# Optimization experiments

Hardware: AMD Instinct MI355X
Metric: run time of the kernel (lower is better)

## Reference

```python
import jax, jax.numpy as jnp
import numpy as np

HIDDEN = 4096
N_HEADS = 32
N_KV = 32
HEAD_DIM = 128
T = 2048
EPS = 1e-5
ROPE_THETA = 1000000.0


def rms_norm(x, w, eps=EPS):
    var = jnp.mean(x * x, axis=-1, keepdims=True)
    return x * jax.lax.rsqrt(var + eps) * w


def apply_rope(x, positions):
    # x: [T, H, D] ; neox-style (rotate halves), full rotary_dim = HEAD_DIM
    half = HEAD_DIM // 2
    inv_freq = 1.0 / (ROPE_THETA ** (jnp.arange(0, half, dtype=jnp.float32) / half))
    ang = positions.astype(jnp.float32)[:, None] * inv_freq  # [T, half]
    cos = jnp.cos(ang)[:, None, :]  # [T, 1, half]
    sin = jnp.sin(ang)[:, None, :]
    x1, x2 = x[..., :half], x[..., half:]
    return jnp.concatenate([x1 * cos - x2 * sin, x2 * cos + x1 * sin], axis=-1)


def setup_inputs() -> dict:
    key = jax.random.key(0)
    ks = jax.random.split(key, 5)
    s = 0.02
    qkv_out = (N_HEADS + 2 * N_KV) * HEAD_DIM
    return {
        "hidden_states": jax.random.normal(ks[0], (T, HIDDEN), jnp.float32),
        "positions": jnp.arange(T, dtype=jnp.int32),
        "w_qkv": jax.random.normal(ks[1], (qkv_out, HIDDEN), jnp.float32) * s,
        "b_qkv": jax.random.normal(ks[2], (qkv_out,), jnp.float32) * s,
        "q_norm_w": jnp.ones((N_HEADS * HEAD_DIM,), jnp.float32),
        "k_norm_w": jnp.ones((N_KV * HEAD_DIM,), jnp.float32),
        "w_o": jax.random.normal(ks[3], (HIDDEN, N_HEADS * HEAD_DIM), jnp.float32) * s,
    }


def reference(hidden_states, positions, w_qkv, b_qkv, q_norm_w, k_norm_w, w_o):
    q_size = N_HEADS * HEAD_DIM
    kv_size = N_KV * HEAD_DIM
    qkv = hidden_states @ w_qkv.T + b_qkv  # [T, q+2kv]
    q, k, v = jnp.split(qkv, [q_size, q_size + kv_size], axis=-1)
    # QK RMSNorm over the full flattened q / k widths (as in Molmo)
    q = rms_norm(q, q_norm_w)
    k = rms_norm(k, k_norm_w)
    q = apply_rope(q.reshape(T, N_HEADS, HEAD_DIM), positions)
    k = apply_rope(k.reshape(T, N_KV, HEAD_DIM), positions)
    v = v.reshape(T, N_KV, HEAD_DIM)
    scale = HEAD_DIM ** -0.5
    scores = jnp.einsum("qhd,khd->hqk", q, k) * scale  # [H, T, T]
    causal = positions[:, None] >= positions[None, :]
    scores = jnp.where(causal[None], scores, jnp.float32(-1e30))
    probs = jax.nn.softmax(scores, axis=-1)
    attn = jnp.einsum("hqk,khd->qhd", probs, v).reshape(T, N_HEADS * HEAD_DIM)
    return attn @ w_o.T
```

## Files before the change

kernel.cpp:

```cpp
#include <hip/hip_runtime.h>
#include <hip/hip_bf16.h>

#define T_SEQ 2048
#define NH 32
#define HD 128
#define QKV_N 12288
#define V_OFF 8192

typedef __bf16 bf16;
typedef __attribute__((ext_vector_type(4))) __bf16 bf16x4;
typedef __attribute__((ext_vector_type(8))) __bf16 bf16x8;
typedef __attribute__((ext_vector_type(4))) float f32x4;

#define GLDS16(g, l)                                                        \
  __builtin_amdgcn_global_load_lds(                                         \
      (const __attribute__((address_space(1))) void*)(g),                   \
      (__attribute__((address_space(3))) void*)(l), 16, 0, 0)

__device__ inline bf16x8 load8(const bf16* p) { return *(const bf16x8*)p; }
__device__ inline bf16x8 load8(const float* p) {
    f32x4 a = *(const f32x4*)p;
    f32x4 b = *(const f32x4*)(p + 4);
    bf16x8 r;
    r[0] = (bf16)a[0]; r[1] = (bf16)a[1]; r[2] = (bf16)a[2]; r[3] = (bf16)a[3];
    r[4] = (bf16)b[0]; r[5] = (bf16)b[1]; r[6] = (bf16)b[2]; r[7] = (bf16)b[3];
    return r;
}

__global__ __launch_bounds__(256)
void f32_to_bf16(const float* __restrict__ in, bf16* __restrict__ out, int n8)
{
    for (int i = blockIdx.x * 256 + threadIdx.x; i < n8; i += gridDim.x * 256)
        *(bf16x8*)(out + (size_t)i * 8) = load8(in + (size_t)i * 8);
}

template <typename TO>
__global__ __launch_bounds__(512, 2)
void gemm_bt_p1(const bf16* __restrict__ A, int lda,
                const bf16* __restrict__ B,
                const float* __restrict__ bias,
                TO* __restrict__ C, int ldc,
                int mTiles, int colPerXcd, int K)
{
    __shared__ char lds[98304];
    char* ldsA = lds;
    char* ldsB = lds + 65536;

    const int tid  = threadIdx.x;
    const int wave = tid >> 6, lane = tid & 63;
    const int quad = lane >> 4, l16 = lane & 15;
    const int wm = wave >> 1, wn = wave & 1;

    const int b   = blockIdx.x;
    const int xcd = b & 7, i = b >> 3;
    const int rowBase = (i % mTiles) * 256;
    const int colBase = (xcd * colPerXcd + i / mTiles) * 128;
    const int nK = K >> 5;

    const bf16* gA0; const bf16* gA1; const bf16* gB0;
    {
        int d0 = tid * 16;
        int s0 = d0 ^ ((d0 >> 3) & 0x70);
        gA0 = A + (size_t)(rowBase + (s0 >> 6)) * lda + ((s0 & 63) >> 1);
        int d1 = (512 + tid) * 16;
        int s1 = d1 ^ ((d1 >> 3) & 0x70);
        gA1 = A + (size_t)(rowBase + (s1 >> 6)) * lda + ((s1 & 63) >> 1);
        int d2 = tid * 16;
        int s2 = d2 ^ ((d2 >> 3) & 0x70);
        gB0 = B + (size_t)(colBase + (s2 >> 6)) * K + ((s2 & 63) >> 1);
    }

    auto stage = [&](int kt) {
        const int sl = kt & 3;
        const int ko = kt * 32;
        GLDS16(gA0 + ko, ldsA + sl * 16384 + wave * 1024);
        GLDS16(gA1 + ko, ldsA + sl * 16384 + 8192 + wave * 1024);
        GLDS16(gB0 + ko, ldsB + sl * 8192 + wave * 1024);
    };

    int offA[4], offB[4];
#pragma unroll
    for (int mi = 0; mi < 4; ++mi) {
        int a = (wm * 64 + mi * 16 + l16) * 64 + quad * 16;
        offA[mi] = a ^ ((a >> 3) & 0x70);
    }
#pragma unroll
    for (int ni = 0; ni < 4; ++ni) {
        int a = (wn * 64 + ni * 16 + l16) * 64 + quad * 16;
        offB[ni] = a ^ ((a >> 3) & 0x70);
    }

    f32x4 acc[4][4] = {};

    stage(0); stage(1); stage(2);
    asm volatile("s_waitcnt vmcnt(6)" ::: "memory");
    __builtin_amdgcn_s_barrier();

#pragma unroll 4
    for (int kt = 0; kt < nK; ++kt) {
        const char* sA = ldsA + (kt & 3) * 16384;
        const char* sB = ldsB + (kt & 3) * 8192;
        bf16x8 af[4], bfr[4];
#pragma unroll
        for (int mi = 0; mi < 4; ++mi) af[mi]  = *(const bf16x8*)(sA + offA[mi]);
#pragma unroll
        for (int ni = 0; ni < 4; ++ni) bfr[ni] = *(const bf16x8*)(sB + offB[ni]);
        if (kt + 3 < nK) stage(kt + 3);
        __builtin_amdgcn_sched_barrier(0);
        __builtin_amdgcn_s_setprio(1);
#pragma unroll
        for (int mi = 0; mi < 4; ++mi)
#pragma unroll
            for (int ni = 0; ni < 4; ++ni)
                acc[mi][ni] = __builtin_amdgcn_mfma_f32_16x16x32_bf16(
                    af[mi], bfr[ni], acc[mi][ni], 0, 0, 0);
        __builtin_amdgcn_s_setprio(0);
        __builtin_amdgcn_sched_barrier(0);
        if (kt + 3 < nK) {
            asm volatile("s_waitcnt vmcnt(6)" ::: "memory");
            __builtin_amdgcn_s_barrier();
        } else if (kt + 2 < nK) {
            asm volatile("s_waitcnt vmcnt(3)" ::: "memory");
            __builtin_amdgcn_s_barrier();
        } else if (kt + 1 < nK) {
            asm volatile("s_waitcnt vmcnt(0)" ::: "memory");
            __builtin_amdgcn_s_barrier();
        }
    }

#pragma unroll
    for (int ni = 0; ni < 4; ++ni) {
        int col = colBase + wn * 64 + ni * 16 + l16;
        float bv = bias ? bias[col] : 0.0f;
#pragma unroll
        for (int mi = 0; mi < 4; ++mi) {
            int row0 = rowBase + wm * 64 + mi * 16 + quad * 4;
#pragma unroll
            for (int r = 0; r < 4; ++r)
                C[(size_t)(row0 + r) * ldc + col] = (TO)(acc[mi][ni][r] + bv);
        }
    }
}

#define BM 128
#define BN 128
#define BK 32

template <typename TA, typename TB, typename TO>
__global__ __launch_bounds__(256, 2)
void gemm_bt_bias(const TA* __restrict__ A, int lda,
                  const TB* __restrict__ B,
                  const float* __restrict__ bias,
                  TO* __restrict__ C, int ldc,
                  int M, int N, int K)
{
    __shared__ bf16 sA[BM * BK];
    __shared__ bf16 sB[BN * BK];
    const int tid  = threadIdx.x;
    const int wave = tid >> 6, lane = tid & 63;
    const int quad = lane >> 4, l16 = lane & 15;
    const int wm = wave >> 1, wn = wave & 1;
    const int rowBase = blockIdx.x * BM;
    const int colBase = blockIdx.y * BN;

    int c0 = wave * 128 + lane;
    int rowA0 = c0 >> 2, kgA0 = c0 & 3;
    int rowA1 = (c0 + 64) >> 2, kgA1 = (c0 + 64) & 3;

    f32x4 acc[4][4] = {};

    for (int k0 = 0; k0 < K; k0 += BK) {
        bf16x8 ra0 = load8(A + (size_t)(rowBase + rowA0) * lda + k0 + kgA0 * 8);
        bf16x8 ra1 = load8(A + (size_t)(rowBase + rowA1) * lda + k0 + kgA1 * 8);
        bf16x8 rb0 = load8(B + (size_t)(colBase + rowA0) * K + k0 + kgA0 * 8);
        bf16x8 rb1 = load8(B + (size_t)(colBase + rowA1) * K + k0 + kgA1 * 8);
        __syncthreads();
        *(bf16x8*)(sA + rowA0 * BK + kgA0 * 8) = ra0;
        *(bf16x8*)(sA + rowA1 * BK + kgA1 * 8) = ra1;
        *(bf16x8*)(sB + rowA0 * BK + kgA0 * 8) = rb0;
        *(bf16x8*)(sB + rowA1 * BK + kgA1 * 8) = rb1;
        __syncthreads();

        bf16x8 af[4], bfr[4];
        for (int mi = 0; mi < 4; ++mi)
            af[mi] = *(const bf16x8*)(sA + (wm * 64 + mi * 16 + l16) * BK + quad * 8);
        for (int ni = 0; ni < 4; ++ni)
            bfr[ni] = *(const bf16x8*)(sB + (wn * 64 + ni * 16 + l16) * BK + quad * 8);
        for (int mi = 0; mi < 4; ++mi)
            for (int ni = 0; ni < 4; ++ni)
                acc[mi][ni] = __builtin_amdgcn_mfma_f32_16x16x32_bf16(
                    af[mi], bfr[ni], acc[mi][ni], 0, 0, 0);
    }

    for (int ni = 0; ni < 4; ++ni) {
        int col = colBase + wn * 64 + ni * 16 + l16;
        float bv = bias ? bias[col] : 0.0f;
        for (int mi = 0; mi < 4; ++mi) {
            int row0 = rowBase + wm * 64 + mi * 16 + quad * 4;
            for (int r = 0; r < 4; ++r)
                C[(size_t)(row0 + r) * ldc + col] = (TO)(acc[mi][ni][r] + bv);
        }
    }
}

__global__ __launch_bounds__(256)
void rmsnorm_rope(bf16* __restrict__ qkv, const float* __restrict__ qw,
                  const float* __restrict__ kw, const int* __restrict__ pos)
{
    const int t   = blockIdx.x;
    const int sel = blockIdx.y;
    bf16* x = qkv + (size_t)t * QKV_N + sel * 4096;
    const float* w = sel ? kw : qw;
    const int tid = threadIdx.x;

    float ss = 0.f;
    {
        int i0 = tid * 16;
        bf16x8 a = *(const bf16x8*)(x + i0);
        bf16x8 b = *(const bf16x8*)(x + i0 + 8);
        for (int j = 0; j < 8; ++j) { float fa = (float)a[j]; ss += fa * fa; }
        for (int j = 0; j < 8; ++j) { float fb = (float)b[j]; ss += fb * fb; }
    }
    for (int off = 1; off < 64; off <<= 1) ss += __shfl_xor(ss, off, 64);
    __shared__ float red[4];
    if ((tid & 63) == 0) red[tid >> 6] = ss;
    __syncthreads();
    float tot = red[0] + red[1] + red[2] + red[3];
    float rstd = rsqrtf(tot * (1.0f / 4096.0f) + 1e-5f);

    float fp = (float)pos[t];
    for (int i = tid; i < 2048; i += 256) {
        int h = i >> 6;
        int d = i & 63;
        int base = h * 128 + d;
        float x1 = (float)x[base]      * rstd * w[base];
        float x2 = (float)x[base + 64] * rstd * w[base + 64];
        float ang = fp * exp2f(-(float)d * 0.31143075889569023f);
        float s, c;
        sincosf(ang, &s, &c);
        x[base]      = (bf16)(x1 * c - x2 * s);
        x[base + 64] = (bf16)(x2 * c + x1 * s);
    }
}

__global__ __launch_bounds__(256)
void v_transpose(const bf16* __restrict__ qkv, bf16* __restrict__ vt)
{
    __shared__ bf16 tile[64][65];
    int t0 = blockIdx.x * 64, d0 = blockIdx.y * 64, h = blockIdx.z;
    int x = threadIdx.x & 63, y4 = threadIdx.x >> 6;
    for (int yy = y4; yy < 64; yy += 4)
        tile[yy][x] = qkv[(size_t)(t0 + yy) * QKV_N + V_OFF + h * HD + d0 + x];
    __syncthreads();
    for (int yy = y4; yy < 64; yy += 4)
        vt[(size_t)(h * HD + d0 + yy) * T_SEQ + t0 + x] = tile[x][yy];
}

#define SKP 136
#define SVP 72
#define PBP 72

__global__ __launch_bounds__(256, 2)
void flash_attn(bf16* qkv, const bf16* vt)
{
    __shared__ bf16 sK[64 * SKP];
    __shared__ bf16 sV[128 * SVP];
    __shared__ bf16 pbuf[4 * 16 * PBP];

    const int tid  = threadIdx.x;
    const int wave = tid >> 6, lane = tid & 63;
    const int quad = lane >> 4, l16 = lane & 15;
    const int h    = blockIdx.y;

    const float sc = 0.08838834764831845f * 1.4426950408889634f;
    bf16* pb = pbuf + wave * 16 * PBP;

    for (int half = 0; half < 2; ++half) {
        const int blk  = half ? (31 - (int)blockIdx.x) : (int)blockIdx.x;
        const int q0w  = blk * 64 + wave * 16;
        const int kend = blk * 64;
        const int qln  = q0w + l16;

        bf16x8 qf[4];
        {
            const bf16* qrow = qkv + (size_t)qln * QKV_N + h * HD;
            for (int c = 0; c < 4; ++c)
                qf[c] = *(const bf16x8*)(qrow + c * 32 + quad * 8);
        }

        f32x4 oacc[8] = {};
        float m2 = -1e30f, lsum = 0.f;

        for (int kb = 0; kb <= kend; kb += 64) {
            __syncthreads();
            for (int j = 0; j < 4; ++j) {
                int c = tid + j * 256;
                int r = c >> 4, off = (c & 15) * 8;
                bf16x8 v = *(const bf16x8*)(qkv + (size_t)(kb + r) * QKV_N + 4096 + h * HD + off);
                *(bf16x8*)(sK + r * SKP + off) = v;
            }
            for (int j = 0; j < 4; ++j) {
                int c = tid + j * 256;
                int d = c >> 3, off = (c & 7) * 8;
                bf16x8 v = *(const bf16x8*)(vt + (size_t)(h * HD + d) * T_SEQ + kb + off);
                *(bf16x8*)(sV + d * SVP + off) = v;
            }
            __syncthreads();

            const int stmax = (kb == kend) ? (wave + 1) : 4;

            f32x4 s[4] = {};
            for (int st = 0; st < 4; ++st) {
                if (st >= stmax) break;
                const bf16* kbase = sK + (st * 16 + l16) * SKP + quad * 8;
                for (int c = 0; c < 4; ++c) {
                    bf16x8 kf = *(const bf16x8*)(kbase + c * 32);
                    s[st] = __builtin_amdgcn_mfma_f32_16x16x32_bf16(kf, qf[c], s[st], 0, 0, 0);
                }
            }
            for (int st = 0; st < 4; ++st) {
                int k0r = kb + st * 16 + quad * 4;
                for (int r = 0; r < 4; ++r) {
                    float v = s[st][r] * sc;
                    s[st][r] = (k0r + r <= qln) ? v : -1e30f;
                }
            }
            float mx = -1e30f;
            for (int st = 0; st < 4; ++st)
                for (int r = 0; r < 4; ++r) mx = fmaxf(mx, s[st][r]);
            mx = fmaxf(mx, __shfl_xor(mx, 16, 64));
            mx = fmaxf(mx, __shfl_xor(mx, 32, 64));
            float mnew  = fmaxf(m2, mx);
            float alpha = exp2f(m2 - mnew);
            float ps = 0.f;
            for (int st = 0; st < 4; ++st)
                for (int r = 0; r < 4; ++r) {
                    float p = exp2f(s[st][r] - mnew);
                    s[st][r] = p;
                    ps += p;
                }
            ps += __shfl_xor(ps, 16, 64);
            ps += __shfl_xor(ps, 32, 64);
            lsum = lsum * alpha + ps;
            m2 = mnew;

            float ar[4];
            for (int r = 0; r < 4; ++r) ar[r] = __shfl(alpha, quad * 4 + r, 64);
            for (int c = 0; c < 8; ++c)
                for (int r = 0; r < 4; ++r) oacc[c][r] *= ar[r];

            for (int st = 0; st < 4; ++st) {
                bf16x4 pw;
                for (int r = 0; r < 4; ++r) pw[r] = (bf16)s[st][r];
                *(bf16x4*)(pb + l16 * PBP + st * 16 + quad * 4) = pw;
            }
            __builtin_amdgcn_s_waitcnt(0xC07F);
            for (int ph = 0; ph < 2; ++ph) {
                bf16x8 pf = *(const bf16x8*)(pb + l16 * PBP + ph * 32 + quad * 8);
                for (int c = 0; c < 8; ++c) {
                    bf16x8 vf = *(const bf16x8*)(sV + (c * 16 + l16) * SVP + ph * 32 + quad * 8);
                    oacc[c] = __builtin_amdgcn_mfma_f32_16x16x32_bf16(pf, vf, oacc[c], 0, 0, 0);
                }
            }
        }

        float lr[4];
        for (int r = 0; r < 4; ++r) lr[r] = __shfl(lsum, quad * 4 + r, 64);
        for (int r = 0; r < 4; ++r) {
            float inv = 1.0f / lr[r];
            int t = q0w + quad * 4 + r;
            for (int c = 0; c < 8; ++c)
                qkv[(size_t)t * QKV_N + V_OFF + h * HD + c * 16 + l16] =
                    (bf16)(oacc[c][r] * inv);
        }
    }
}

extern "C" void kernel_launch(void* const* d_in, const int* in_sizes, int n_in,
                              void* d_out, int out_size, void* d_ws, size_t ws_size,
                              hipStream_t stream)
{
    const float* hidden   = (const float*)d_in[0];
    const int*   pos      = (const int*)d_in[1];
    const float* w_qkv    = (const float*)d_in[2];
    const float* b_qkv    = (const float*)d_in[3];
    const float* q_norm_w = (const float*)d_in[4];
    const float* k_norm_w = (const float*)d_in[5];
    const float* w_o      = (const float*)d_in[6];
    float* out = (float*)d_out;

    bf16* qkv = (bf16*)d_ws;
    bf16* vt  = qkv + (size_t)T_SEQ * QKV_N;
    bf16* wqb = vt  + (size_t)4096 * T_SEQ;
    bf16* wob = wqb + (size_t)QKV_N * 4096;
    bf16* hib = wob + (size_t)4096 * 4096;
    const size_t need = ((size_t)T_SEQ * QKV_N + (size_t)4096 * T_SEQ +
                         (size_t)QKV_N * 4096 + (size_t)4096 * 4096 +
                         (size_t)T_SEQ * 4096) * 2;

    if (ws_size >= need) {
        f32_to_bf16<<<2048, 256, 0, stream>>>(hidden, hib, T_SEQ * 4096 / 8);
        f32_to_bf16<<<8192, 256, 0, stream>>>(w_qkv, wqb, QKV_N * 4096 / 8);
        f32_to_bf16<<<4096, 256, 0, stream>>>(w_o, wob, 4096 * 4096 / 8);

        gemm_bt_p1<bf16><<<768, 512, 0, stream>>>(
            hib, 4096, wqb, b_qkv, qkv, QKV_N, 8, 12, 4096);
        rmsnorm_rope<<<dim3(T_SEQ, 2), 256, 0, stream>>>(qkv, q_norm_w, k_norm_w, pos);
        v_transpose<<<dim3(T_SEQ / 64, 2, NH), 256, 0, stream>>>(qkv, vt);
        flash_attn<<<dim3(T_SEQ / 128, NH), 256, 0, stream>>>(qkv, vt);
        gemm_bt_p1<float><<<256, 512, 0, stream>>>(
            qkv + V_OFF, QKV_N, wob, nullptr, out, 4096, 8, 4, 4096);
    } else {
        gemm_bt_bias<float, float, bf16><<<dim3(T_SEQ / BM, QKV_N / BN), 256, 0, stream>>>(
            hidden, 4096, w_qkv, b_qkv, qkv, QKV_N, T_SEQ, QKV_N, 4096);
        rmsnorm_rope<<<dim3(T_SEQ, 2), 256, 0, stream>>>(qkv, q_norm_w, k_norm_w, pos);
        v_transpose<<<dim3(T_SEQ / 64, 2, NH), 256, 0, stream>>>(qkv, vt);
        flash_attn<<<dim3(T_SEQ / 128, NH), 256, 0, stream>>>(qkv, vt);
        gemm_bt_bias<bf16, float, float><<<dim3(T_SEQ / BM, 4096 / BN), 256, 0, stream>>>(
            qkv + V_OFF, QKV_N, w_o, nullptr, out, 4096, T_SEQ, 4096, 4096);
    }
}
```

Measured before the change: 798.0 us.

## Shrink GEMM tile to 128x128 with 256 threads and double-buffered LDS

Replaces the 256x128-tile, 512-thread GEMM with a 4-stage LDS pipeline by a 128x128-tile, 256-thread kernel with 2-stage double buffering and 32KB LDS. Launch bounds and grid sizes change so more blocks run, giving 1536 and 512 blocks and up to 3 blocks per CU. The aim is better occupancy and CU coverage, especially for the smaller output projection, at the price of less data reuse per tile and a shallower prefetch that may expose more memory latency.

```diff
diff --git a/kernel.cpp b/kernel.cpp
--- a/kernel.cpp
+++ b/kernel.cpp
@@ -35,16 +35,14 @@
 }
 
 template <typename TO>
-__global__ __launch_bounds__(512, 2)
-void gemm_bt_p1(const bf16* __restrict__ A, int lda,
+__global__ __launch_bounds__(256, 3)
+void gemm_bt_cr(const bf16* __restrict__ A, int lda,
                 const bf16* __restrict__ B,
                 const float* __restrict__ bias,
                 TO* __restrict__ C, int ldc,
                 int mTiles, int colPerXcd, int K)
 {
-    __shared__ char lds[98304];
-    char* ldsA = lds;
-    char* ldsB = lds + 65536;
+    __shared__ char lds[32768];
 
     const int tid  = threadIdx.x;
     const int wave = tid >> 6, lane = tid & 63;
@@ -53,29 +51,29 @@
 
     const int b   = blockIdx.x;
     const int xcd = b & 7, i = b >> 3;
-    const int rowBase = (i % mTiles) * 256;
+    const int rowBase = (i % mTiles) * 128;
     const int colBase = (xcd * colPerXcd + i / mTiles) * 128;
     const int nK = K >> 5;
 
-    const bf16* gA0; const bf16* gA1; const bf16* gB0;
-    {
-        int d0 = tid * 16;
-        int s0 = d0 ^ ((d0 >> 3) & 0x70);
-        gA0 = A + (size_t)(rowBase + (s0 >> 6)) * lda + ((s0 & 63) >> 1);
-        int d1 = (512 + tid) * 16;
-        int s1 = d1 ^ ((d1 >> 3) & 0x70);
-        gA1 = A + (size_t)(rowBase + (s1 >> 6)) * lda + ((s1 & 63) >> 1);
-        int d2 = tid * 16;
-        int s2 = d2 ^ ((d2 >> 3) & 0x70);
-        gB0 = B + (size_t)(colBase + (s2 >> 6)) * K + ((s2 & 63) >> 1);
+    const bf16* gA[2];
+    const bf16* gB[2];
+#pragma unroll
+    for (int j = 0; j < 2; ++j) {
+        int d = (j * 256 + tid) * 16;
+        int s = d ^ ((d >> 3) & 0x70);
+        int row = s >> 6, ke = (s & 63) >> 1;
+        gA[j] = A + (size_t)(rowBase + row) * lda + ke;
+        gB[j] = B + (size_t)(colBase + row) * K + ke;
     }
 
     auto stage = [&](int kt) {
-        const int sl = kt & 3;
+        const int sl = kt & 1;
         const int ko = kt * 32;
-        GLDS16(gA0 + ko, ldsA + sl * 16384 + wave * 1024);
-        GLDS16(gA1 + ko, ldsA + sl * 16384 + 8192 + wave * 1024);
-        GLDS16(gB0 + ko, ldsB + sl * 8192 + wave * 1024);
+#pragma unroll
+        for (int j = 0; j < 2; ++j) {
+            GLDS16(gA[j] + ko, lds + sl * 8192 + j * 4096 + wave * 1024);
+            GLDS16(gB[j] + ko, lds + 16384 + sl * 8192 + j * 4096 + wave * 1024);
+        }
     };
 
     int offA[4], offB[4];
@@ -92,20 +90,20 @@
 
     f32x4 acc[4][4] = {};
 
-    stage(0); stage(1); stage(2);
-    asm volatile("s_waitcnt vmcnt(6)" ::: "memory");
+    stage(0);
+    asm volatile("s_waitcnt vmcnt(0)" ::: "memory");
     __builtin_amdgcn_s_barrier();
 
-#pragma unroll 4
+#pragma unroll 2
     for (int kt = 0; kt < nK; ++kt) {
-        const char* sA = ldsA + (kt & 3) * 16384;
-        const char* sB = ldsB + (kt & 3) * 8192;
+        const char* sA = lds + (kt & 1) * 8192;
+        const char* sB = lds + 16384 + (kt & 1) * 8192;
         bf16x8 af[4], bfr[4];
 #pragma unroll
         for (int mi = 0; mi < 4; ++mi) af[mi]  = *(const bf16x8*)(sA + offA[mi]);
 #pragma unroll
         for (int ni = 0; ni < 4; ++ni) bfr[ni] = *(const bf16x8*)(sB + offB[ni]);
-        if (kt + 3 < nK) stage(kt + 3);
+        if (kt + 1 < nK) stage(kt + 1);
         __builtin_amdgcn_sched_barrier(0);
         __builtin_amdgcn_s_setprio(1);
 #pragma unroll
@@ -116,13 +114,7 @@
                     af[mi], bfr[ni], acc[mi][ni], 0, 0, 0);
         __builtin_amdgcn_s_setprio(0);
         __builtin_amdgcn_sched_barrier(0);
-        if (kt + 3 < nK) {
-            asm volatile("s_waitcnt vmcnt(6)" ::: "memory");
-            __builtin_amdgcn_s_barrier();
-        } else if (kt + 2 < nK) {
-            asm volatile("s_waitcnt vmcnt(3)" ::: "memory");
-            __builtin_amdgcn_s_barrier();
-        } else if (kt + 1 < nK) {
+        if (kt + 1 < nK) {
             asm volatile("s_waitcnt vmcnt(0)" ::: "memory");
             __builtin_amdgcn_s_barrier();
         }
@@ -403,13 +395,13 @@
         f32_to_bf16<<<8192, 256, 0, stream>>>(w_qkv, wqb, QKV_N * 4096 / 8);
         f32_to_bf16<<<4096, 256, 0, stream>>>(w_o, wob, 4096 * 4096 / 8);
 
-        gemm_bt_p1<bf16><<<768, 512, 0, stream>>>(
-            hib, 4096, wqb, b_qkv, qkv, QKV_N, 8, 12, 4096);
+        gemm_bt_cr<bf16><<<1536, 256, 0, stream>>>(
+            hib, 4096, wqb, b_qkv, qkv, QKV_N, 16, 12, 4096);
         rmsnorm_rope<<<dim3(T_SEQ, 2), 256, 0, stream>>>(qkv, q_norm_w, k_norm_w, pos);
         v_transpose<<<dim3(T_SEQ / 64, 2, NH), 256, 0, stream>>>(qkv, vt);
         flash_attn<<<dim3(T_SEQ / 128, NH), 256, 0, stream>>>(qkv, vt);
-        gemm_bt_p1<float><<<256, 512, 0, stream>>>(
-            qkv + V_OFF, QKV_N, wob, nullptr, out, 4096, 8, 4, 4096);
+        gemm_bt_cr<float><<<512, 256, 0, stream>>>(
+            qkv + V_OFF, QKV_N, wob, nullptr, out, 4096, 16, 4, 4096);
     } else {
         gemm_bt_bias<float, float, bf16><<<dim3(T_SEQ / BM, QKV_N / BN), 256, 0, stream>>>(
             hidden, 4096, w_qkv, b_qkv, qkv, QKV_N, T_SEQ, QKV_N, 4096);
```

New measurement: 818.5 us. +2.6%, slower.
